# Kernel tuning notes

Measured on AMD Instinct MI355X. Metric: run time of the kernel, lower is better.

The kernel has to match this reference:

```python
import jax, jax.numpy as jnp
import numpy as np

TOPK = 2


def setup_inputs() -> dict:
    key = jax.random.key(0)
    k1, k2 = jax.random.split(key)
    B, N, D, E, C = 4, 2048, 2048, 8, 512
    token_inputs = jax.random.normal(k1, (B, N, D), dtype=jnp.float32)
    # bottleneck_in.weight.t() stacked over experts: [E, D, C]; scaled like a real init
    bottleneck_weights = jax.random.normal(k2, (E, D, C), dtype=jnp.float32) * 0.02
    return {
        "token_inputs": token_inputs,
        "bottleneck_weights": bottleneck_weights,
        "expert_capacity": 640,
    }


def _routing(router_probs, expert_capacity, topk):
    # router_probs: [B, N, E]
    B, N, E = router_probs.shape
    _, expert_indices = jax.lax.top_k(router_probs, topk)      # [B, N, topk]
    idx = jnp.transpose(expert_indices, (0, 2, 1)).reshape(B, topk * N)
    expert_mask = jax.nn.one_hot(idx, E, dtype=jnp.int32)       # [B, topk*N, E]
    token_priority = jnp.cumsum(expert_mask, axis=1) * expert_mask - 1
    token_priority = token_priority.reshape(B, topk, N, E)
    token_priority = jnp.transpose(token_priority, (0, 2, 1, 3))  # [B, N, topk, E]
    token_priority = jnp.max(token_priority, axis=2)              # [B, N, E]
    # one-hot over capacity; negative (-1) and >= capacity priorities map to all-zero rows
    cap_range = jnp.arange(expert_capacity, dtype=jnp.int32)
    dispatch = (token_priority[..., None] == cap_range).astype(jnp.float32)  # [B,N,E,C]
    combine = router_probs[..., None] * dispatch                            # [B,N,E,C]
    return dispatch, combine


def reference(token_inputs, bottleneck_weights, expert_capacity):
    # activation_cache: [B, N, E, Cb]
    activation_cache = jnp.einsum("bnd,edc->bnec", token_inputs, bottleneck_weights)
    router_logits = jnp.sqrt(jnp.sum(activation_cache * activation_cache, axis=-1))  # [B,N,E]
    router_probs = jax.nn.softmax(router_logits, axis=-1)
    dispatch, combine = _routing(router_probs, expert_capacity, TOPK)
    return jnp.stack([dispatch, combine], axis=0)  # [2, B, N, E, capacity]
```

## Files before the change

### kernel.cpp

```cpp
#include <hip/hip_runtime.h>
#include <math.h>

constexpr int Bb = 4, Nn = 2048, Dd = 2048, Ee = 8, Cbn = 512;
constexpr int Mm = Bb * Nn;

typedef _Float16 half8 __attribute__((ext_vector_type(8)));
typedef float floatx16 __attribute__((ext_vector_type(16)));

#define GLL16(g, l)                                                     \
  __builtin_amdgcn_global_load_lds(                                     \
      (const __attribute__((address_space(1))) void*)(g),               \
      (__attribute__((address_space(3))) void*)(l), 16, 0, 0)

__global__ __launch_bounds__(256) void transpose_w(const float* __restrict__ W,
                                                   _Float16* __restrict__ WThi,
                                                   _Float16* __restrict__ WTlo) {
  const int kt = blockIdx.x;
  const int ct = blockIdx.y;
  const int e = blockIdx.z;
  __shared__ _Float16 thi[64][72];
  __shared__ _Float16 tlo[64][72];
  const int tx = threadIdx.x & 15, ty = threadIdx.x >> 4;
  const float* src = W + ((size_t)(e * 2048 + kt * 64)) * 512 + ct * 64;
#pragma unroll
  for (int p = 0; p < 4; ++p) {
    int kk = ty + p * 16;
    float4 v = *(const float4*)(src + (size_t)kk * 512 + tx * 4);
    _Float16 h;
    h = (_Float16)v.x; thi[tx * 4 + 0][kk] = h; tlo[tx * 4 + 0][kk] = (_Float16)(v.x - (float)h);
    h = (_Float16)v.y; thi[tx * 4 + 1][kk] = h; tlo[tx * 4 + 1][kk] = (_Float16)(v.y - (float)h);
    h = (_Float16)v.z; thi[tx * 4 + 2][kk] = h; tlo[tx * 4 + 2][kk] = (_Float16)(v.z - (float)h);
    h = (_Float16)v.w; thi[tx * 4 + 3][kk] = h; tlo[tx * 4 + 3][kk] = (_Float16)(v.w - (float)h);
  }
  __syncthreads();
  const int rr = threadIdx.x >> 3;
  const int ch = threadIdx.x & 7;
  _Float16* dh = WThi + ((size_t)(e * 512 + ct * 64)) * 2048 + kt * 64;
  _Float16* dl = WTlo + ((size_t)(e * 512 + ct * 64)) * 2048 + kt * 64;
#pragma unroll
  for (int p = 0; p < 2; ++p) {
    int cc = rr + p * 32;
    *(half8*)(dh + (size_t)cc * 2048 + ch * 8) = *(const half8*)(&thi[cc][ch * 8]);
    *(half8*)(dl + (size_t)cc * 2048 + ch * 8) = *(const half8*)(&tlo[cc][ch * 8]);
  }
}

__global__ __launch_bounds__(256) void gemm_mfma(const float* __restrict__ X,
                                                 const _Float16* __restrict__ WThi,
                                                 const _Float16* __restrict__ WTlo,
                                                 float* __restrict__ partial) {
  const int bid = blockIdx.x;
  const int st = bid >> 8;
  const int stm = st & 3;
  const int stn = st >> 2;
  const int li = bid & 255;
  const int mtile = stm * 16 + (li >> 4);
  const int ntile = stn * 16 + (li & 15);

  const int tid = threadIdx.x;
  const int wave = tid >> 6, lane = tid & 63;
  const int wm = wave >> 1, wn = wave & 1;
  const int h = lane >> 5;

  __shared__ __align__(16) char lds[32768];
  char* ldsA = lds;
  char* ldsBhi = lds + 16384;
  char* ldsBlo = lds + 24576;

  const int lrA = lane >> 3;
  const int cposA = lane & 7;
  const int cgA = cposA ^ lrA;
  const float* xg[4];
  int ldsAoff[4];
#pragma unroll
  for (int q = 0; q < 4; ++q) {
    const int row = wave * 32 + q * 8 + lrA;
    xg[q] = X + (size_t)(mtile * 128 + row) * 2048 + cgA * 4;
    ldsAoff[q] = (wave * 32 + q * 8) * 128;
  }

  const int lrB = lane >> 2;
  const int cposB = lane & 3;
  const int cgB = cposB ^ ((lrB >> 1) & 3);
  const int rB0s = wave * 32 + lrB;
  const int rB1s = rB0s + 16;
  const _Float16* wh0 = WThi + (size_t)(ntile * 128 + rB0s) * 2048 + cgB * 8;
  const _Float16* wh1 = WThi + (size_t)(ntile * 128 + rB1s) * 2048 + cgB * 8;
  const _Float16* wl0 = WTlo + (size_t)(ntile * 128 + rB0s) * 2048 + cgB * 8;
  const _Float16* wl1 = WTlo + (size_t)(ntile * 128 + rB1s) * 2048 + cgB * 8;
  const int lqB0 = wave * 2048;
  const int lqB1 = lqB0 + 1024;

  const int keyA = lane & 7;
  const int rowA0 = wm * 64 + (lane & 31);
  const int rowA1 = rowA0 + 32;
  int oAf0[2][2], oAf1[2][2];
#pragma unroll
  for (int s = 0; s < 2; ++s)
#pragma unroll
    for (int c = 0; c < 2; ++c) {
      const int g = s * 4 + h * 2 + c;
      oAf0[s][c] = rowA0 * 128 + ((g ^ keyA) << 4);
      oAf1[s][c] = rowA1 * 128 + ((g ^ keyA) << 4);
    }

  const int rB0 = wn * 64 + (lane & 31);
  const int rB1 = rB0 + 32;
  auto foffB = [&](int r, int s) {
    return r * 64 + (((s * 2 + h) ^ ((r >> 1) & 3)) << 4);
  };
  const int oB0[2] = {foffB(rB0, 0), foffB(rB0, 1)};
  const int oB1[2] = {foffB(rB1, 0), foffB(rB1, 1)};

  floatx16 acc00 = {}, acc01 = {}, acc10 = {}, acc11 = {};

  auto cvtA = [](const char* p0, const char* p1, half8& ah, half8& al) {
    float4 f0 = *(const float4*)p0;
    float4 f1 = *(const float4*)p1;
    float xf[8] = {f0.x, f0.y, f0.z, f0.w, f1.x, f1.y, f1.z, f1.w};
#pragma unroll
    for (int j = 0; j < 8; ++j) {
      _Float16 hv = (_Float16)xf[j];
      ah[j] = hv;
      al[j] = (_Float16)(xf[j] - (float)hv);
    }
  };

  for (int kt = 0; kt < 64; ++kt) {
    const int k0 = kt * 32;
#pragma unroll
    for (int q = 0; q < 4; ++q) GLL16(xg[q] + k0, ldsA + ldsAoff[q]);
    GLL16(wh0 + k0, ldsBhi + lqB0);
    GLL16(wh1 + k0, ldsBhi + lqB1);
    GLL16(wl0 + k0, ldsBlo + lqB0);
    GLL16(wl1 + k0, ldsBlo + lqB1);
    __syncthreads();
#pragma unroll
    for (int s = 0; s < 2; ++s) {
      half8 ah0, al0, ah1, al1;
      cvtA(ldsA + oAf0[s][0], ldsA + oAf0[s][1], ah0, al0);
      cvtA(ldsA + oAf1[s][0], ldsA + oAf1[s][1], ah1, al1);
      half8 bh0 = *(const half8*)(ldsBhi + oB0[s]);
      half8 bh1 = *(const half8*)(ldsBhi + oB1[s]);
      half8 bl0 = *(const half8*)(ldsBlo + oB0[s]);
      half8 bl1 = *(const half8*)(ldsBlo + oB1[s]);
      acc00 = __builtin_amdgcn_mfma_f32_32x32x16_f16(ah0, bh0, acc00, 0, 0, 0);
      acc00 = __builtin_amdgcn_mfma_f32_32x32x16_f16(ah0, bl0, acc00, 0, 0, 0);
      acc00 = __builtin_amdgcn_mfma_f32_32x32x16_f16(al0, bh0, acc00, 0, 0, 0);
      acc01 = __builtin_amdgcn_mfma_f32_32x32x16_f16(ah0, bh1, acc01, 0, 0, 0);
      acc01 = __builtin_amdgcn_mfma_f32_32x32x16_f16(ah0, bl1, acc01, 0, 0, 0);
      acc01 = __builtin_amdgcn_mfma_f32_32x32x16_f16(al0, bh1, acc01, 0, 0, 0);
      acc10 = __builtin_amdgcn_mfma_f32_32x32x16_f16(ah1, bh0, acc10, 0, 0, 0);
      acc10 = __builtin_amdgcn_mfma_f32_32x32x16_f16(ah1, bl0, acc10, 0, 0, 0);
      acc10 = __builtin_amdgcn_mfma_f32_32x32x16_f16(al1, bh0, acc10, 0, 0, 0);
      acc11 = __builtin_amdgcn_mfma_f32_32x32x16_f16(ah1, bh1, acc11, 0, 0, 0);
      acc11 = __builtin_amdgcn_mfma_f32_32x32x16_f16(ah1, bl1, acc11, 0, 0, 0);
      acc11 = __builtin_amdgcn_mfma_f32_32x32x16_f16(al1, bh1, acc11, 0, 0, 0);
    }
    __syncthreads();
  }

  float myv = 0.f;
#pragma unroll
  for (int i = 0; i < 2; ++i) {
    const floatx16& c0 = i ? acc10 : acc00;
    const floatx16& c1 = i ? acc11 : acc01;
#pragma unroll
    for (int reg = 0; reg < 16; ++reg) {
      float v = c0[reg] * c0[reg] + c1[reg] * c1[reg];
#pragma unroll
      for (int m = 1; m <= 16; m <<= 1) v += __shfl_xor(v, m, 64);
      if ((lane & 31) == i * 16 + reg) myv = v;
    }
  }
  {
    const int i = (lane & 31) >> 4;
    const int reg = lane & 15;
    const int row = i * 32 + (reg & 3) + 8 * (reg >> 2) + 4 * h;
    const int token = mtile * 128 + wm * 64 + row;
    const int slice = ntile * 2 + wn;
    partial[(size_t)token * 64 + slice] = myv;
  }
}

__global__ __launch_bounds__(256) void scan_route(const float* __restrict__ partial,
                                                  int* __restrict__ ig,
                                                  float* __restrict__ p1g,
                                                  float* __restrict__ p2g,
                                                  int* __restrict__ prios) {
  const int b = blockIdx.x;
  const int tid = threadIdx.x;
  __shared__ unsigned char sI1[Nn];
  __shared__ unsigned char sI2[Nn];
  __shared__ int cnts[256][8];

  for (int i = 0; i < 8; ++i) {
    const int tl = i * 256 + tid;
    const int t = b * Nn + tl;
    float l[Ee];
    float mx = -1e30f;
#pragma unroll
    for (int e = 0; e < Ee; ++e) {
      float s = 0.f;
#pragma unroll
      for (int u = 0; u < 8; ++u) s += partial[(size_t)t * 64 + e * 8 + u];
      l[e] = sqrtf(s);
      mx = fmaxf(mx, l[e]);
    }
    float sum = 0.f, pe[Ee];
#pragma unroll
    for (int e = 0; e < Ee; ++e) {
      pe[e] = expf(l[e] - mx);
      sum += pe[e];
    }
    float inv = 1.f / sum;
    int i1 = 0;
    float b1 = l[0];
#pragma unroll
    for (int e = 1; e < Ee; ++e)
      if (l[e] > b1) { b1 = l[e]; i1 = e; }
    int i2 = -1;
    float b2 = -1e30f;
#pragma unroll
    for (int e = 0; e < Ee; ++e)
      if (e != i1 && l[e] > b2) { b2 = l[e]; i2 = e; }
    sI1[tl] = (unsigned char)i1;
    sI2[tl] = (unsigned char)i2;
    ig[t] = i1 | (i2 << 8);
    p1g[t] = pe[i1] * inv;
    p2g[t] = pe[i2] * inv;
  }
  __syncthreads();

  int cnt[8] = {0, 0, 0, 0, 0, 0, 0, 0};
  int eloc[16];
  const int base_p = tid * 16;
#pragma unroll
  for (int i = 0; i < 16; ++i) {
    int pp = base_p + i;
    int k = pp >> 11;
    int n = pp & (Nn - 1);
    int e = k == 0 ? (int)sI1[n] : (int)sI2[n];
    eloc[i] = e;
    cnt[e]++;
  }
#pragma unroll
  for (int e = 0; e < 8; ++e) cnts[tid][e] = cnt[e];
  __syncthreads();
  if (tid < 8) {
    int run = 0;
    for (int i = 0; i < 256; ++i) {
      int v = cnts[i][tid];
      cnts[i][tid] = run;
      run += v;
    }
  }
  __syncthreads();
  int base[8];
#pragma unroll
  for (int e = 0; e < 8; ++e) base[e] = cnts[tid][e];
#pragma unroll
  for (int i = 0; i < 16; ++i) {
    int e = eloc[i];
    prios[b * 2 * Nn + base_p + i] = base[e]++;
  }
}

__global__ __launch_bounds__(256) void out_kernel(const int* __restrict__ ig,
                                                  const float* __restrict__ p1g,
                                                  const float* __restrict__ p2g,
                                                  const int* __restrict__ prios,
                                                  float* __restrict__ out, int cap) {
  const int t = blockIdx.x;
  const int tid = threadIdx.x;
  const int b = t >> 11, n = t & (Nn - 1);
  const int pair = ig[t];
  const int e1 = pair & 0xff, e2 = (pair >> 8) & 0xff;
  const int q1 = prios[b * 2 * Nn + n];
  const int q2 = prios[b * 2 * Nn + Nn + n];
  const float v1 = p1g[t], v2 = p2g[t];
  const int g1 = (q1 < cap) ? e1 * cap + q1 : -1;
  const int g2 = (q2 < cap) ? e2 * cap + q2 : -1;
  const int row4 = Ee * cap / 4;
  float4* drow = (float4*)out + (size_t)t * row4;
  float4* crow = drow + (size_t)Mm * row4;
  for (int f = tid; f < row4; f += 256) {
    float4 d = make_float4(0.f, 0.f, 0.f, 0.f);
    float4 c = make_float4(0.f, 0.f, 0.f, 0.f);
    const int base = f * 4;
    if (g1 >= base && g1 < base + 4) {
      ((float*)&d)[g1 - base] = 1.f;
      ((float*)&c)[g1 - base] = v1;
    }
    if (g2 >= base && g2 < base + 4) {
      ((float*)&d)[g2 - base] = 1.f;
      ((float*)&c)[g2 - base] = v2;
    }
    drow[f] = d;
    crow[f] = c;
  }
}

extern "C" void kernel_launch(void* const* d_in, const int* in_sizes, int n_in,
                              void* d_out, int out_size, void* d_ws, size_t ws_size,
                              hipStream_t stream) {
  const float* X = (const float*)d_in[0];
  const float* W = (const float*)d_in[1];
  float* out = (float*)d_out;
  const int cap = out_size / (2 * Bb * Nn * Ee);

  char* ws = (char*)d_ws;
  _Float16* WThi = (_Float16*)ws;
  _Float16* WTlo = (_Float16*)(ws + 16777216ull);
  float* partial = (float*)(ws + 33554432ull);
  int* ig = (int*)(ws + 35651584ull);
  float* p1g = (float*)(ig + Mm);
  float* p2g = p1g + Mm;
  int* prios = (int*)(p2g + Mm);

  transpose_w<<<dim3(32, 8, 8), 256, 0, stream>>>(W, WThi, WTlo);
  gemm_mfma<<<2048, 256, 0, stream>>>(X, WThi, WTlo, partial);
  scan_route<<<Bb, 256, 0, stream>>>(partial, ig, p1g, p2g, prios);
  out_kernel<<<Mm, 256, 0, stream>>>(ig, p1g, p2g, prios, out, cap);
}
```

Baseline: 824.4 us.

## Fuse four kernels into one persistent kernel with grid barriers

Merges the weight transpose/split, the MFMA GEMM, the routing scan and the output write into one persistent kernel of 512 blocks that loops over the original tiles and separates the phases with atomic-counter grid barriers. This removes three kernel launches and their inter-kernel gaps. In exchange the grid is smaller (4 GEMM tiles per block, a hipMemsetAsync is added), and the spin barriers rely on all 512 blocks being co-resident, so the kernel deadlocks if they are not. The routing phase still runs on only 4 blocks while all the others wait.

```diff
diff --git a/kernel.cpp b/kernel.cpp
--- a/kernel.cpp
+++ b/kernel.cpp
@@ -3,6 +3,7 @@
 
 constexpr int Bb = 4, Nn = 2048, Dd = 2048, Ee = 8, Cbn = 512;
 constexpr int Mm = Bb * Nn;
+constexpr int NBLK = 512;
 
 typedef _Float16 half8 __attribute__((ext_vector_type(8)));
 typedef float floatx16 __attribute__((ext_vector_type(16)));
@@ -12,292 +13,308 @@
       (const __attribute__((address_space(1))) void*)(g),               \
       (__attribute__((address_space(3))) void*)(l), 16, 0, 0)
 
-__global__ __launch_bounds__(256) void transpose_w(const float* __restrict__ W,
-                                                   _Float16* __restrict__ WThi,
-                                                   _Float16* __restrict__ WTlo) {
-  const int kt = blockIdx.x;
-  const int ct = blockIdx.y;
-  const int e = blockIdx.z;
-  __shared__ _Float16 thi[64][72];
-  __shared__ _Float16 tlo[64][72];
-  const int tx = threadIdx.x & 15, ty = threadIdx.x >> 4;
-  const float* src = W + ((size_t)(e * 2048 + kt * 64)) * 512 + ct * 64;
-#pragma unroll
-  for (int p = 0; p < 4; ++p) {
-    int kk = ty + p * 16;
-    float4 v = *(const float4*)(src + (size_t)kk * 512 + tx * 4);
-    _Float16 h;
-    h = (_Float16)v.x; thi[tx * 4 + 0][kk] = h; tlo[tx * 4 + 0][kk] = (_Float16)(v.x - (float)h);
-    h = (_Float16)v.y; thi[tx * 4 + 1][kk] = h; tlo[tx * 4 + 1][kk] = (_Float16)(v.y - (float)h);
-    h = (_Float16)v.z; thi[tx * 4 + 2][kk] = h; tlo[tx * 4 + 2][kk] = (_Float16)(v.z - (float)h);
-    h = (_Float16)v.w; thi[tx * 4 + 3][kk] = h; tlo[tx * 4 + 3][kk] = (_Float16)(v.w - (float)h);
-  }
+__device__ inline void grid_barrier(int* cnt) {
   __syncthreads();
-  const int rr = threadIdx.x >> 3;
-  const int ch = threadIdx.x & 7;
-  _Float16* dh = WThi + ((size_t)(e * 512 + ct * 64)) * 2048 + kt * 64;
-  _Float16* dl = WTlo + ((size_t)(e * 512 + ct * 64)) * 2048 + kt * 64;
-#pragma unroll
-  for (int p = 0; p < 2; ++p) {
-    int cc = rr + p * 32;
-    *(half8*)(dh + (size_t)cc * 2048 + ch * 8) = *(const half8*)(&thi[cc][ch * 8]);
-    *(half8*)(dl + (size_t)cc * 2048 + ch * 8) = *(const half8*)(&tlo[cc][ch * 8]);
-  }
+  if (threadIdx.x == 0) {
+    __threadfence();
+    atomicAdd(cnt, 1);
+    while (__hip_atomic_load(cnt, __ATOMIC_ACQUIRE, __HIP_MEMORY_SCOPE_AGENT) <
+           NBLK) {
+    }
+  }
+  __syncthreads();
 }
 
-__global__ __launch_bounds__(256) void gemm_mfma(const float* __restrict__ X,
-                                                 const _Float16* __restrict__ WThi,
-                                                 const _Float16* __restrict__ WTlo,
-                                                 float* __restrict__ partial) {
-  const int bid = blockIdx.x;
-  const int st = bid >> 8;
-  const int stm = st & 3;
-  const int stn = st >> 2;
-  const int li = bid & 255;
-  const int mtile = stm * 16 + (li >> 4);
-  const int ntile = stn * 16 + (li & 15);
-
+__global__ __launch_bounds__(256, 2) void mega(
+    const float* __restrict__ X, const float* __restrict__ W,
+    _Float16* __restrict__ WThi, _Float16* __restrict__ WTlo,
+    float* __restrict__ partial, int* __restrict__ ig,
+    float* __restrict__ p1g, float* __restrict__ p2g, int* __restrict__ prios,
+    int* __restrict__ bar, float* __restrict__ out, int cap) {
+  __shared__ __align__(16) char smem[32768];
   const int tid = threadIdx.x;
-  const int wave = tid >> 6, lane = tid & 63;
-  const int wm = wave >> 1, wn = wave & 1;
-  const int h = lane >> 5;
-
-  __shared__ __align__(16) char lds[32768];
-  char* ldsA = lds;
-  char* ldsBhi = lds + 16384;
-  char* ldsBlo = lds + 24576;
-
-  const int lrA = lane >> 3;
-  const int cposA = lane & 7;
-  const int cgA = cposA ^ lrA;
-  const float* xg[4];
-  int ldsAoff[4];
-#pragma unroll
-  for (int q = 0; q < 4; ++q) {
-    const int row = wave * 32 + q * 8 + lrA;
-    xg[q] = X + (size_t)(mtile * 128 + row) * 2048 + cgA * 4;
-    ldsAoff[q] = (wave * 32 + q * 8) * 128;
-  }
-
-  const int lrB = lane >> 2;
-  const int cposB = lane & 3;
-  const int cgB = cposB ^ ((lrB >> 1) & 3);
-  const int rB0s = wave * 32 + lrB;
-  const int rB1s = rB0s + 16;
-  const _Float16* wh0 = WThi + (size_t)(ntile * 128 + rB0s) * 2048 + cgB * 8;
-  const _Float16* wh1 = WThi + (size_t)(ntile * 128 + rB1s) * 2048 + cgB * 8;
-  const _Float16* wl0 = WTlo + (size_t)(ntile * 128 + rB0s) * 2048 + cgB * 8;
-  const _Float16* wl1 = WTlo + (size_t)(ntile * 128 + rB1s) * 2048 + cgB * 8;
-  const int lqB0 = wave * 2048;
-  const int lqB1 = lqB0 + 1024;
-
-  const int keyA = lane & 7;
-  const int rowA0 = wm * 64 + (lane & 31);
-  const int rowA1 = rowA0 + 32;
-  int oAf0[2][2], oAf1[2][2];
-#pragma unroll
-  for (int s = 0; s < 2; ++s)
-#pragma unroll
-    for (int c = 0; c < 2; ++c) {
-      const int g = s * 4 + h * 2 + c;
-      oAf0[s][c] = rowA0 * 128 + ((g ^ keyA) << 4);
-      oAf1[s][c] = rowA1 * 128 + ((g ^ keyA) << 4);
-    }
-
-  const int rB0 = wn * 64 + (lane & 31);
-  const int rB1 = rB0 + 32;
-  auto foffB = [&](int r, int s) {
-    return r * 64 + (((s * 2 + h) ^ ((r >> 1) & 3)) << 4);
-  };
-  const int oB0[2] = {foffB(rB0, 0), foffB(rB0, 1)};
-  const int oB1[2] = {foffB(rB1, 0), foffB(rB1, 1)};
-
-  floatx16 acc00 = {}, acc01 = {}, acc10 = {}, acc11 = {};
-
-  auto cvtA = [](const char* p0, const char* p1, half8& ah, half8& al) {
-    float4 f0 = *(const float4*)p0;
-    float4 f1 = *(const float4*)p1;
-    float xf[8] = {f0.x, f0.y, f0.z, f0.w, f1.x, f1.y, f1.z, f1.w};
-#pragma unroll
-    for (int j = 0; j < 8; ++j) {
-      _Float16 hv = (_Float16)xf[j];
-      ah[j] = hv;
-      al[j] = (_Float16)(xf[j] - (float)hv);
-    }
-  };
-
-  for (int kt = 0; kt < 64; ++kt) {
-    const int k0 = kt * 32;
-#pragma unroll
-    for (int q = 0; q < 4; ++q) GLL16(xg[q] + k0, ldsA + ldsAoff[q]);
-    GLL16(wh0 + k0, ldsBhi + lqB0);
-    GLL16(wh1 + k0, ldsBhi + lqB1);
-    GLL16(wl0 + k0, ldsBlo + lqB0);
-    GLL16(wl1 + k0, ldsBlo + lqB1);
+
+  {
+    _Float16(*thi)[72] = (_Float16(*)[72])smem;
+    _Float16(*tlo)[72] = (_Float16(*)[72])(smem + 9216);
+    const int tx = tid & 15, ty = tid >> 4;
+    for (int i = 0; i < 4; ++i) {
+      __syncthreads();
+      const int T = blockIdx.x * 4 + i;
+      const int kt = T & 31, ct = (T >> 5) & 7, e = T >> 8;
+      const float* src = W + ((size_t)(e * 2048 + kt * 64)) * 512 + ct * 64;
+#pragma unroll
+      for (int p = 0; p < 4; ++p) {
+        int kk = ty + p * 16;
+        float4 v = *(const float4*)(src + (size_t)kk * 512 + tx * 4);
+        _Float16 h;
+        h = (_Float16)v.x; thi[tx * 4 + 0][kk] = h; tlo[tx * 4 + 0][kk] = (_Float16)(v.x - (float)h);
+        h = (_Float16)v.y; thi[tx * 4 + 1][kk] = h; tlo[tx * 4 + 1][kk] = (_Float16)(v.y - (float)h);
+        h = (_Float16)v.z; thi[tx * 4 + 2][kk] = h; tlo[tx * 4 + 2][kk] = (_Float16)(v.z - (float)h);
+        h = (_Float16)v.w; thi[tx * 4 + 3][kk] = h; tlo[tx * 4 + 3][kk] = (_Float16)(v.w - (float)h);
+      }
+      __syncthreads();
+      const int rr = tid >> 3;
+      const int ch = tid & 7;
+      _Float16* dh = WThi + ((size_t)(e * 512 + ct * 64)) * 2048 + kt * 64;
+      _Float16* dl = WTlo + ((size_t)(e * 512 + ct * 64)) * 2048 + kt * 64;
+#pragma unroll
+      for (int p = 0; p < 2; ++p) {
+        int cc = rr + p * 32;
+        *(half8*)(dh + (size_t)cc * 2048 + ch * 8) = *(const half8*)(&thi[cc][ch * 8]);
+        *(half8*)(dl + (size_t)cc * 2048 + ch * 8) = *(const half8*)(&tlo[cc][ch * 8]);
+      }
+    }
+  }
+  grid_barrier(bar + 0);
+
+  {
+    char* ldsA = smem;
+    char* ldsBhi = smem + 16384;
+    char* ldsBlo = smem + 24576;
+
+    const int wave = tid >> 6, lane = tid & 63;
+    const int wm = wave >> 1, wn = wave & 1;
+    const int h = lane >> 5;
+
+    const int lrA = lane >> 3;
+    const int cposA = lane & 7;
+    const int cgA = cposA ^ lrA;
+    int ldsAoff[4];
+#pragma unroll
+    for (int q = 0; q < 4; ++q) ldsAoff[q] = (wave * 32 + q * 8) * 128;
+
+    const int lrB = lane >> 2;
+    const int cposB = lane & 3;
+    const int cgB = cposB ^ ((lrB >> 1) & 3);
+    const int lqB0 = wave * 2048;
+    const int lqB1 = lqB0 + 1024;
+
+    const int keyA = lane & 7;
+    const int rowA0 = wm * 64 + (lane & 31);
+    const int rowA1 = rowA0 + 32;
+    int oAf0[2][2], oAf1[2][2];
+#pragma unroll
+    for (int s = 0; s < 2; ++s)
+#pragma unroll
+      for (int c = 0; c < 2; ++c) {
+        const int g = s * 4 + h * 2 + c;
+        oAf0[s][c] = rowA0 * 128 + ((g ^ keyA) << 4);
+        oAf1[s][c] = rowA1 * 128 + ((g ^ keyA) << 4);
+      }
+
+    const int rB0 = wn * 64 + (lane & 31);
+    const int rB1 = rB0 + 32;
+    auto foffB = [&](int r, int s) {
+      return r * 64 + (((s * 2 + h) ^ ((r >> 1) & 3)) << 4);
+    };
+    const int oB0[2] = {foffB(rB0, 0), foffB(rB0, 1)};
+    const int oB1[2] = {foffB(rB1, 0), foffB(rB1, 1)};
+
+    auto cvtA = [](const char* p0, const char* p1, half8& ah, half8& al) {
+      float4 f0 = *(const float4*)p0;
+      float4 f1 = *(const float4*)p1;
+      float xf[8] = {f0.x, f0.y, f0.z, f0.w, f1.x, f1.y, f1.z, f1.w};
+#pragma unroll
+      for (int j = 0; j < 8; ++j) {
+        _Float16 hv = (_Float16)xf[j];
+        ah[j] = hv;
+        al[j] = (_Float16)(xf[j] - (float)hv);
+      }
+    };
+
+    for (int j = 0; j < 4; ++j) {
+      const int bid = blockIdx.x * 4 + j;
+      const int st = bid >> 8;
+      const int stm = st & 3;
+      const int stn = st >> 2;
+      const int li = bid & 255;
+      const int mtile = stm * 16 + (li >> 4);
+      const int ntile = stn * 16 + (li & 15);
+
+      const float* xg[4];
+#pragma unroll
+      for (int q = 0; q < 4; ++q) {
+        const int row = wave * 32 + q * 8 + lrA;
+        xg[q] = X + (size_t)(mtile * 128 + row) * 2048 + cgA * 4;
+      }
+      const int rB0s = wave * 32 + lrB;
+      const int rB1s = rB0s + 16;
+      const _Float16* wh0 = WThi + (size_t)(ntile * 128 + rB0s) * 2048 + cgB * 8;
+      const _Float16* wh1 = WThi + (size_t)(ntile * 128 + rB1s) * 2048 + cgB * 8;
+      const _Float16* wl0 = WTlo + (size_t)(ntile * 128 + rB0s) * 2048 + cgB * 8;
+      const _Float16* wl1 = WTlo + (size_t)(ntile * 128 + rB1s) * 2048 + cgB * 8;
+
+      floatx16 acc00 = {}, acc01 = {}, acc10 = {}, acc11 = {};
+
+      __syncthreads();
+      for (int kt = 0; kt < 64; ++kt) {
+        const int k0 = kt * 32;
+#pragma unroll
+        for (int q = 0; q < 4; ++q) GLL16(xg[q] + k0, ldsA + ldsAoff[q]);
+        GLL16(wh0 + k0, ldsBhi + lqB0);
+        GLL16(wh1 + k0, ldsBhi + lqB1);
+        GLL16(wl0 + k0, ldsBlo + lqB0);
+        GLL16(wl1 + k0, ldsBlo + lqB1);
+        __syncthreads();
+#pragma unroll
+        for (int s = 0; s < 2; ++s) {
+          half8 ah0, al0, ah1, al1;
+          cvtA(ldsA + oAf0[s][0], ldsA + oAf0[s][1], ah0, al0);
+          cvtA(ldsA + oAf1[s][0], ldsA + oAf1[s][1], ah1, al1);
+          half8 bh0 = *(const half8*)(ldsBhi + oB0[s]);
+          half8 bh1 = *(const half8*)(ldsBhi + oB1[s]);
+          half8 bl0 = *(const half8*)(ldsBlo + oB0[s]);
+          half8 bl1 = *(const half8*)(ldsBlo + oB1[s]);
+          acc00 = __builtin_amdgcn_mfma_f32_32x32x16_f16(ah0, bh0, acc00, 0, 0, 0);
+          acc00 = __builtin_amdgcn_mfma_f32_32x32x16_f16(ah0, bl0, acc00, 0, 0, 0);
+          acc00 = __builtin_amdgcn_mfma_f32_32x32x16_f16(al0, bh0, acc00, 0, 0, 0);
+          acc01 = __builtin_amdgcn_mfma_f32_32x32x16_f16(ah0, bh1, acc01, 0, 0, 0);
+          acc01 = __builtin_amdgcn_mfma_f32_32x32x16_f16(ah0, bl1, acc01, 0, 0, 0);
+          acc01 = __builtin_amdgcn_mfma_f32_32x32x16_f16(al0, bh1, acc01, 0, 0, 0);
+          acc10 = __builtin_amdgcn_mfma_f32_32x32x16_f16(ah1, bh0, acc10, 0, 0, 0);
+          acc10 = __builtin_amdgcn_mfma_f32_32x32x16_f16(ah1, bl0, acc10, 0, 0, 0);
+          acc10 = __builtin_amdgcn_mfma_f32_32x32x16_f16(al1, bh0, acc10, 0, 0, 0);
+          acc11 = __builtin_amdgcn_mfma_f32_32x32x16_f16(ah1, bh1, acc11, 0, 0, 0);
+          acc11 = __builtin_amdgcn_mfma_f32_32x32x16_f16(ah1, bl1, acc11, 0, 0, 0);
+          acc11 = __builtin_amdgcn_mfma_f32_32x32x16_f16(al1, bh1, acc11, 0, 0, 0);
+        }
+        __syncthreads();
+      }
+
+      float myv = 0.f;
+#pragma unroll
+      for (int i = 0; i < 2; ++i) {
+        const floatx16& c0 = i ? acc10 : acc00;
+        const floatx16& c1 = i ? acc11 : acc01;
+#pragma unroll
+        for (int reg = 0; reg < 16; ++reg) {
+          float v = c0[reg] * c0[reg] + c1[reg] * c1[reg];
+#pragma unroll
+          for (int m = 1; m <= 16; m <<= 1) v += __shfl_xor(v, m, 64);
+          if ((lane & 31) == i * 16 + reg) myv = v;
+        }
+      }
+      {
+        const int i = (lane & 31) >> 4;
+        const int reg = lane & 15;
+        const int row = i * 32 + (reg & 3) + 8 * (reg >> 2) + 4 * h;
+        const int token = mtile * 128 + wm * 64 + row;
+        const int slice = ntile * 2 + wn;
+        partial[(size_t)token * 64 + slice] = myv;
+      }
+    }
+  }
+  grid_barrier(bar + 1);
+
+  if (blockIdx.x < Bb) {
+    const int b = blockIdx.x;
+    unsigned char* sI1 = (unsigned char*)smem;
+    unsigned char* sI2 = (unsigned char*)(smem + 2048);
+    int(*cnts)[8] = (int(*)[8])(smem + 4096);
+    for (int i = 0; i < 8; ++i) {
+      const int tl = i * 256 + tid;
+      const int t = b * Nn + tl;
+      float l[Ee];
+      float mx = -1e30f;
+#pragma unroll
+      for (int e = 0; e < Ee; ++e) {
+        float s = 0.f;
+#pragma unroll
+        for (int u = 0; u < 8; ++u) s += partial[(size_t)t * 64 + e * 8 + u];
+        l[e] = sqrtf(s);
+        mx = fmaxf(mx, l[e]);
+      }
+      float sum = 0.f, pe[Ee];
+#pragma unroll
+      for (int e = 0; e < Ee; ++e) {
+        pe[e] = expf(l[e] - mx);
+        sum += pe[e];
+      }
+      float inv = 1.f / sum;
+      int i1 = 0;
+      float b1 = l[0];
+#pragma unroll
+      for (int e = 1; e < Ee; ++e)
+        if (l[e] > b1) { b1 = l[e]; i1 = e; }
+      int i2 = -1;
+      float b2 = -1e30f;
+#pragma unroll
+      for (int e = 0; e < Ee; ++e)
+        if (e != i1 && l[e] > b2) { b2 = l[e]; i2 = e; }
+      sI1[tl] = (unsigned char)i1;
+      sI2[tl] = (unsigned char)i2;
+      ig[t] = i1 | (i2 << 8);
+      p1g[t] = pe[i1] * inv;
+      p2g[t] = pe[i2] * inv;
+    }
     __syncthreads();
-#pragma unroll
-    for (int s = 0; s < 2; ++s) {
-      half8 ah0, al0, ah1, al1;
-      cvtA(ldsA + oAf0[s][0], ldsA + oAf0[s][1], ah0, al0);
-      cvtA(ldsA + oAf1[s][0], ldsA + oAf1[s][1], ah1, al1);
-      half8 bh0 = *(const half8*)(ldsBhi + oB0[s]);
-      half8 bh1 = *(const half8*)(ldsBhi + oB1[s]);
-      half8 bl0 = *(const half8*)(ldsBlo + oB0[s]);
-      half8 bl1 = *(const half8*)(ldsBlo + oB1[s]);
-      acc00 = __builtin_amdgcn_mfma_f32_32x32x16_f16(ah0, bh0, acc00, 0, 0, 0);
-      acc00 = __builtin_amdgcn_mfma_f32_32x32x16_f16(ah0, bl0, acc00, 0, 0, 0);
-      acc00 = __builtin_amdgcn_mfma_f32_32x32x16_f16(al0, bh0, acc00, 0, 0, 0);
-      acc01 = __builtin_amdgcn_mfma_f32_32x32x16_f16(ah0, bh1, acc01, 0, 0, 0);
-      acc01 = __builtin_amdgcn_mfma_f32_32x32x16_f16(ah0, bl1, acc01, 0, 0, 0);
-      acc01 = __builtin_amdgcn_mfma_f32_32x32x16_f16(al0, bh1, acc01, 0, 0, 0);
-      acc10 = __builtin_amdgcn_mfma_f32_32x32x16_f16(ah1, bh0, acc10, 0, 0, 0);
-      acc10 = __builtin_amdgcn_mfma_f32_32x32x16_f16(ah1, bl0, acc10, 0, 0, 0);
-      acc10 = __builtin_amdgcn_mfma_f32_32x32x16_f16(al1, bh0, acc10, 0, 0, 0);
-      acc11 = __builtin_amdgcn_mfma_f32_32x32x16_f16(ah1, bh1, acc11, 0, 0, 0);
-      acc11 = __builtin_amdgcn_mfma_f32_32x32x16_f16(ah1, bl1, acc11, 0, 0, 0);
-      acc11 = __builtin_amdgcn_mfma_f32_32x32x16_f16(al1, bh1, acc11, 0, 0, 0);
-    }
+    int cnt[8] = {0, 0, 0, 0, 0, 0, 0, 0};
+    int eloc[16];
+    const int base_p = tid * 16;
+#pragma unroll
+    for (int i = 0; i < 16; ++i) {
+      int pp = base_p + i;
+      int k = pp >> 11;
+      int n = pp & (Nn - 1);
+      int e = k == 0 ? (int)sI1[n] : (int)sI2[n];
+      eloc[i] = e;
+      cnt[e]++;
+    }
+#pragma unroll
+    for (int e = 0; e < 8; ++e) cnts[tid][e] = cnt[e];
     __syncthreads();
-  }
-
-  float myv = 0.f;
-#pragma unroll
-  for (int i = 0; i < 2; ++i) {
-    const floatx16& c0 = i ? acc10 : acc00;
-    const floatx16& c1 = i ? acc11 : acc01;
-#pragma unroll
-    for (int reg = 0; reg < 16; ++reg) {
-      float v = c0[reg] * c0[reg] + c1[reg] * c1[reg];
-#pragma unroll
-      for (int m = 1; m <= 16; m <<= 1) v += __shfl_xor(v, m, 64);
-      if ((lane & 31) == i * 16 + reg) myv = v;
-    }
-  }
+    if (tid < 8) {
+      int run = 0;
+      for (int i = 0; i < 256; ++i) {
+        int v = cnts[i][tid];
+        cnts[i][tid] = run;
+        run += v;
+      }
+    }
+    __syncthreads();
+    int base[8];
+#pragma unroll
+    for (int e = 0; e < 8; ++e) base[e] = cnts[tid][e];
+#pragma unroll
+    for (int i = 0; i < 16; ++i) {
+      int e = eloc[i];
+      prios[b * 2 * Nn + base_p + i] = base[e]++;
+    }
+  }
+  grid_barrier(bar + 2);
+
   {
-    const int i = (lane & 31) >> 4;
-    const int reg = lane & 15;
-    const int row = i * 32 + (reg & 3) + 8 * (reg >> 2) + 4 * h;
-    const int token = mtile * 128 + wm * 64 + row;
-    const int slice = ntile * 2 + wn;
-    partial[(size_t)token * 64 + slice] = myv;
-  }
-}
-
-__global__ __launch_bounds__(256) void scan_route(const float* __restrict__ partial,
-                                                  int* __restrict__ ig,
-                                                  float* __restrict__ p1g,
-                                                  float* __restrict__ p2g,
-                                                  int* __restrict__ prios) {
-  const int b = blockIdx.x;
-  const int tid = threadIdx.x;
-  __shared__ unsigned char sI1[Nn];
-  __shared__ unsigned char sI2[Nn];
-  __shared__ int cnts[256][8];
-
-  for (int i = 0; i < 8; ++i) {
-    const int tl = i * 256 + tid;
-    const int t = b * Nn + tl;
-    float l[Ee];
-    float mx = -1e30f;
-#pragma unroll
-    for (int e = 0; e < Ee; ++e) {
-      float s = 0.f;
-#pragma unroll
-      for (int u = 0; u < 8; ++u) s += partial[(size_t)t * 64 + e * 8 + u];
-      l[e] = sqrtf(s);
-      mx = fmaxf(mx, l[e]);
-    }
-    float sum = 0.f, pe[Ee];
-#pragma unroll
-    for (int e = 0; e < Ee; ++e) {
-      pe[e] = expf(l[e] - mx);
-      sum += pe[e];
-    }
-    float inv = 1.f / sum;
-    int i1 = 0;
-    float b1 = l[0];
-#pragma unroll
-    for (int e = 1; e < Ee; ++e)
-      if (l[e] > b1) { b1 = l[e]; i1 = e; }
-    int i2 = -1;
-    float b2 = -1e30f;
-#pragma unroll
-    for (int e = 0; e < Ee; ++e)
-      if (e != i1 && l[e] > b2) { b2 = l[e]; i2 = e; }
-    sI1[tl] = (unsigned char)i1;
-    sI2[tl] = (unsigned char)i2;
-    ig[t] = i1 | (i2 << 8);
-    p1g[t] = pe[i1] * inv;
-    p2g[t] = pe[i2] * inv;
-  }
-  __syncthreads();
-
-  int cnt[8] = {0, 0, 0, 0, 0, 0, 0, 0};
-  int eloc[16];
-  const int base_p = tid * 16;
-#pragma unroll
-  for (int i = 0; i < 16; ++i) {
-    int pp = base_p + i;
-    int k = pp >> 11;
-    int n = pp & (Nn - 1);
-    int e = k == 0 ? (int)sI1[n] : (int)sI2[n];
-    eloc[i] = e;
-    cnt[e]++;
-  }
-#pragma unroll
-  for (int e = 0; e < 8; ++e) cnts[tid][e] = cnt[e];
-  __syncthreads();
-  if (tid < 8) {
-    int run = 0;
-    for (int i = 0; i < 256; ++i) {
-      int v = cnts[i][tid];
-      cnts[i][tid] = run;
-      run += v;
-    }
-  }
-  __syncthreads();
-  int base[8];
-#pragma unroll
-  for (int e = 0; e < 8; ++e) base[e] = cnts[tid][e];
-#pragma unroll
-  for (int i = 0; i < 16; ++i) {
-    int e = eloc[i];
-    prios[b * 2 * Nn + base_p + i] = base[e]++;
-  }
-}
-
-__global__ __launch_bounds__(256) void out_kernel(const int* __restrict__ ig,
-                                                  const float* __restrict__ p1g,
-                                                  const float* __restrict__ p2g,
-                                                  const int* __restrict__ prios,
-                                                  float* __restrict__ out, int cap) {
-  const int t = blockIdx.x;
-  const int tid = threadIdx.x;
-  const int b = t >> 11, n = t & (Nn - 1);
-  const int pair = ig[t];
-  const int e1 = pair & 0xff, e2 = (pair >> 8) & 0xff;
-  const int q1 = prios[b * 2 * Nn + n];
-  const int q2 = prios[b * 2 * Nn + Nn + n];
-  const float v1 = p1g[t], v2 = p2g[t];
-  const int g1 = (q1 < cap) ? e1 * cap + q1 : -1;
-  const int g2 = (q2 < cap) ? e2 * cap + q2 : -1;
-  const int row4 = Ee * cap / 4;
-  float4* drow = (float4*)out + (size_t)t * row4;
-  float4* crow = drow + (size_t)Mm * row4;
-  for (int f = tid; f < row4; f += 256) {
-    float4 d = make_float4(0.f, 0.f, 0.f, 0.f);
-    float4 c = make_float4(0.f, 0.f, 0.f, 0.f);
-    const int base = f * 4;
-    if (g1 >= base && g1 < base + 4) {
-      ((float*)&d)[g1 - base] = 1.f;
-      ((float*)&c)[g1 - base] = v1;
-    }
-    if (g2 >= base && g2 < base + 4) {
-      ((float*)&d)[g2 - base] = 1.f;
-      ((float*)&c)[g2 - base] = v2;
-    }
-    drow[f] = d;
-    crow[f] = c;
+    const int row4 = Ee * 640 / 4;
+    for (int i = 0; i < 16; ++i) {
+      const int t = blockIdx.x * 16 + i;
+      const int b = t >> 11, n = t & (Nn - 1);
+      const int pair = ig[t];
+      const int e1 = pair & 0xff, e2 = (pair >> 8) & 0xff;
+      const int q1 = prios[b * 2 * Nn + n];
+      const int q2 = prios[b * 2 * Nn + Nn + n];
+      const float v1 = p1g[t], v2 = p2g[t];
+      const int g1 = (q1 < cap) ? e1 * cap + q1 : -1;
+      const int g2 = (q2 < cap) ? e2 * cap + q2 : -1;
+      float4* drow = (float4*)out + (size_t)t * (Ee * cap / 4);
+      float4* crow = drow + (size_t)Mm * (Ee * cap / 4);
+      for (int f = tid; f < Ee * cap / 4; f += 256) {
+        float4 d = make_float4(0.f, 0.f, 0.f, 0.f);
+        float4 c = make_float4(0.f, 0.f, 0.f, 0.f);
+        const int base = f * 4;
+        if (g1 >= base && g1 < base + 4) {
+          ((float*)&d)[g1 - base] = 1.f;
+          ((float*)&c)[g1 - base] = v1;
+        }
+        if (g2 >= base && g2 < base + 4) {
+          ((float*)&d)[g2 - base] = 1.f;
+          ((float*)&c)[g2 - base] = v2;
+        }
+        drow[f] = d;
+        crow[f] = c;
+      }
+    }
+    (void)row4;
   }
 }
 
@@ -314,12 +331,12 @@
   _Float16* WTlo = (_Float16*)(ws + 16777216ull);
   float* partial = (float*)(ws + 33554432ull);
   int* ig = (int*)(ws + 35651584ull);
-  float* p1g = (float*)(ig + Mm);
-  float* p2g = p1g + Mm;
-  int* prios = (int*)(p2g + Mm);
-
-  transpose_w<<<dim3(32, 8, 8), 256, 0, stream>>>(W, WThi, WTlo);
-  gemm_mfma<<<2048, 256, 0, stream>>>(X, WThi, WTlo, partial);
-  scan_route<<<Bb, 256, 0, stream>>>(partial, ig, p1g, p2g, prios);
-  out_kernel<<<Mm, 256, 0, stream>>>(ig, p1g, p2g, prios, out, cap);
+  float* p1g = (float*)(ws + 35684352ull);
+  float* p2g = (float*)(ws + 35717120ull);
+  int* prios = (int*)(ws + 35749888ull);
+  int* bar = (int*)(ws + 35815424ull);
+
+  hipMemsetAsync(bar, 0, 256, stream);
+  mega<<<NBLK, 256, 0, stream>>>(X, W, WThi, WTlo, partial, ig, p1g, p2g,
+                                 prios, bar, out, cap);
 }
```

After: 1.290 ms. 56.5% more time.
